# Optimization experiments

Hardware: AMD Instinct MI355X
Metric: run time of the kernel (lower is better)

## Reference

```python
import jax, jax.numpy as jnp
import numpy as np
from jax import lax

FS = 5
BL = np.array([1.46, 1.53, 1.33], np.float32)
BA = (np.pi - np.deg2rad(np.array([122.2, 111.9, 116.2]))).astype(np.float32)
A_SIN = (BL * np.sin(BA)).astype(np.float32)   # bond_length * sin(bond_angle)
A_COS = (BL * np.cos(BA)).astype(np.float32)   # bond_length * cos(bond_angle)
INIT_POS = np.array([[-np.sqrt(0.5), np.sqrt(1.5), 0.0],
                     [-np.sqrt(2.0), 0.0, 0.0],
                     [0.0, 0.0, 0.0]], np.float32)


def _rotation(pos):
    # pos: (..., 3 points, 3 coords); builds rot with columns (m_hat, n_hat x m_hat, n_hat)
    m0 = pos[..., 1, :] - pos[..., 0, :]
    m1 = pos[..., 2, :] - pos[..., 1, :]
    m_hat = m1 / (jnp.linalg.norm(m1, axis=-1, keepdims=True) + 1e-16)
    n = jnp.cross(m0, m_hat)
    n_hat = n / (jnp.linalg.norm(n, axis=-1, keepdims=True) + 1e-16)
    c = jnp.cross(n_hat, m_hat)
    return jnp.stack([m_hat, c, n_hat], axis=-1)


def _fragment_access(indices_np, fs=FS):
    # exact translation of PositionLookup.fragment index math (host-side, int constants)
    uniq, counts = np.unique(indices_np, return_counts=True)
    pad = (counts + fs - 1) // fs * fs
    last_pad = pad - counts
    off = np.roll(last_pad, 1)
    off[0] = 0
    off = np.repeat(off, counts)
    access = np.arange(counts.sum()) + off
    return access, int(pad.sum())


def _forward(torsions, access, P):
    # to_snr: (N,3) torsions -> (N, 3 atoms, 3 coords) local spherical points
    x = jnp.broadcast_to(jnp.asarray(A_COS), torsions.shape)
    points = jnp.stack([x, jnp.cos(torsions) * A_SIN, jnp.sin(torsions) * A_SIN], axis=-1)
    # fragment: scatter residues into padded per-chain slots
    padded = jnp.zeros((P, 3, 3), points.dtype).at[access].set(points)
    F = P // FS
    atom = padded.reshape(F, FS * 3, 3)          # (F, 15, 3) local snr points
    # stage 1: 15 sequential NeRF extension steps, vectorized over fragments
    pos0 = jnp.broadcast_to(jnp.asarray(INIT_POS), (F, 3, 3))
    def step(pos, d):                            # pos (F,3,3) last 3 atoms, d (F,3)
        rot = _rotation(pos)
        new = jnp.einsum('fij,fj->fi', rot, d) + pos[:, -1]
        return jnp.concatenate([pos[:, 1:], new[:, None]], axis=1), new
    _, atoms = lax.scan(step, pos0, jnp.swapaxes(atom, 0, 1))
    local = jnp.swapaxes(atoms, 0, 1)            # (F, 15, 3) fragment-local coords
    # stage 2: stitch fragments. Original right-to-left loop == exclusive prefix
    # composition of rigid transforms T_i built from fragment i's last 3 local atoms.
    rot_all = _rotation(local[:, -3:, :])        # (F,3,3)
    t_all = local[:, -1, :]                      # (F,3)
    eye = jnp.eye(3, dtype=local.dtype)[None]
    Rs = jnp.concatenate([eye, rot_all[:-1]], axis=0)
    ts = jnp.concatenate([jnp.zeros((1, 3), local.dtype), t_all[:-1]], axis=0)
    def combine(a, b):                           # (a o b)(x) = Ra(Rb x + tb) + ta
        Ra, ta = a
        Rb, tb = b
        return jnp.einsum('fij,fjk->fik', Ra, Rb), jnp.einsum('fij,fj->fi', Ra, tb) + ta
    Rp, tp = lax.associative_scan(combine, (Rs, ts))
    glob = jnp.einsum('fij,faj->fai', Rp, local) + tp[:, None, :]
    flat = glob.reshape(-1, 3)
    flat = flat - flat[:1]
    residues = flat.reshape(-1, 3, 3)            # (P//... , 3 atoms, 3 coords)
    return residues[jnp.asarray(access)]         # stitch: (N, 3, 3)


def setup_inputs():
    key = jax.random.key(0)
    n_chains, chain_len = 512, 2050              # chain_len % 5 == 0 -> zero padding
    N = n_chains * chain_len
    k1, _ = jax.random.split(key)
    torsions = jax.random.uniform(k1, (N, 3), jnp.float32, -np.pi, np.pi)
    indices = jnp.repeat(jnp.arange(n_chains, dtype=jnp.int32), chain_len)
    return {"torsions": torsions, "indices": indices}


def reference(torsions, indices):
    access, P = _fragment_access(np.asarray(indices))
    return _forward(torsions, access, P)
```

## Files before the change

kernel.cpp:

```cpp
#include <hip/hip_runtime.h>
#include <math.h>


struct Params {
    float as0, as1, as2;
    float ac0, ac1, ac2;
    float ip[9];
};

struct V3 { float x, y, z; };

__device__ __forceinline__ V3 v3(float x, float y, float z) { V3 r; r.x=x; r.y=y; r.z=z; return r; }
__device__ __forceinline__ V3 vsub(V3 a, V3 b) { return v3(a.x-b.x, a.y-b.y, a.z-b.z); }
__device__ __forceinline__ V3 vcross(V3 a, V3 b) {
    return v3(a.y*b.z - a.z*b.y, a.z*b.x - a.x*b.z, a.x*b.y - a.y*b.x);
}
__device__ __forceinline__ float vdot(V3 a, V3 b) { return a.x*b.x + a.y*b.y + a.z*b.z; }

struct Xform {
    float r[9];
    float t[3];
};

__device__ __forceinline__ Xform xf_identity() {
    Xform x;
    x.r[0]=1.f; x.r[1]=0.f; x.r[2]=0.f;
    x.r[3]=0.f; x.r[4]=1.f; x.r[5]=0.f;
    x.r[6]=0.f; x.r[7]=0.f; x.r[8]=1.f;
    x.t[0]=0.f; x.t[1]=0.f; x.t[2]=0.f;
    return x;
}

__device__ __forceinline__ Xform xf_compose(const Xform& a, const Xform& b) {
    Xform c;
#pragma unroll
    for (int i = 0; i < 3; ++i) {
#pragma unroll
        for (int j = 0; j < 3; ++j) {
            c.r[i*3+j] = a.r[i*3+0]*b.r[0*3+j] + a.r[i*3+1]*b.r[1*3+j] + a.r[i*3+2]*b.r[2*3+j];
        }
        c.t[i] = a.r[i*3+0]*b.t[0] + a.r[i*3+1]*b.t[1] + a.r[i*3+2]*b.t[2] + a.t[i];
    }
    return c;
}

__device__ __forceinline__ Xform xf_shfl_up(const Xform& x, int off) {
    Xform y;
#pragma unroll
    for (int i = 0; i < 9; ++i) y.r[i] = __shfl_up(x.r[i], off, 64);
#pragma unroll
    for (int i = 0; i < 3; ++i) y.t[i] = __shfl_up(x.t[i], off, 64);
    return y;
}
__device__ __forceinline__ Xform xf_shfl_down(const Xform& x, int off) {
    Xform y;
#pragma unroll
    for (int i = 0; i < 9; ++i) y.r[i] = __shfl_down(x.r[i], off, 64);
#pragma unroll
    for (int i = 0; i < 3; ++i) y.t[i] = __shfl_down(x.t[i], off, 64);
    return y;
}

#define LSTRIDE 13

__device__ __forceinline__ void xf_to_lds(float* p, const Xform& x) {
#pragma unroll
    for (int i = 0; i < 9; ++i) p[i] = x.r[i];
#pragma unroll
    for (int i = 0; i < 3; ++i) p[9+i] = x.t[i];
}
__device__ __forceinline__ Xform xf_from_lds(const float* p) {
    Xform x;
#pragma unroll
    for (int i = 0; i < 9; ++i) x.r[i] = p[i];
#pragma unroll
    for (int i = 0; i < 3; ++i) x.t[i] = p[9+i];
    return x;
}

__device__ __forceinline__ void xf_store_g(float* g, const Xform& x) {
    float4* q = (float4*)g;
    q[0] = make_float4(x.r[0], x.r[1], x.r[2], x.r[3]);
    q[1] = make_float4(x.r[4], x.r[5], x.r[6], x.r[7]);
    q[2] = make_float4(x.r[8], x.t[0], x.t[1], x.t[2]);
}
__device__ __forceinline__ Xform xf_load_g(const float* g) {
    const float4* q = (const float4*)g;
    float4 a = q[0], b = q[1], c = q[2];
    Xform x;
    x.r[0]=a.x; x.r[1]=a.y; x.r[2]=a.z; x.r[3]=a.w;
    x.r[4]=b.x; x.r[5]=b.y; x.r[6]=b.z; x.r[7]=b.w;
    x.r[8]=c.x; x.t[0]=c.y; x.t[1]=c.z; x.t[2]=c.w;
    return x;
}

__device__ __forceinline__ void fast_sincos(float t, float& s, float& c) {
    const float r = t * 0.15915494309189535f;
    s = __builtin_amdgcn_sinf(r);
    c = __builtin_amdgcn_cosf(r);
}

__device__ __forceinline__ void rot_cols(V3 p0, V3 p1, V3 p2, V3& mh, V3& cc, V3& nh) {
    V3 m0 = vsub(p1, p0);
    V3 m1 = vsub(p2, p1);
    float im = __builtin_amdgcn_rsqf(vdot(m1, m1));
    mh = v3(m1.x*im, m1.y*im, m1.z*im);
    V3 n = vcross(m0, mh);
    float il = __builtin_amdgcn_rsqf(vdot(n, n));
    nh = v3(n.x*il, n.y*il, n.z*il);
    cc = vcross(nh, mh);
}

template <bool STORE>
__device__ __forceinline__ void build_fragment(const float* __restrict__ tf, const Params& prm,
                                               V3* atoms, V3& q0, V3& q1, V3& q2) {
    V3 p0 = v3(prm.ip[0], prm.ip[1], prm.ip[2]);
    V3 p1 = v3(prm.ip[3], prm.ip[4], prm.ip[5]);
    V3 p2 = v3(prm.ip[6], prm.ip[7], prm.ip[8]);
    const float AS[3] = {prm.as0, prm.as1, prm.as2};
    const float AC[3] = {prm.ac0, prm.ac1, prm.ac2};
#pragma unroll
    for (int a = 0; a < 15; ++a) {
        const int j = a % 3;
        float s, c;
        fast_sincos(tf[a], s, c);
        V3 d = v3(AC[j], c * AS[j], s * AS[j]);
        V3 mh, cc, nh;
        rot_cols(p0, p1, p2, mh, cc, nh);
        V3 np;
        np.x = d.x*mh.x + d.y*cc.x + d.z*nh.x + p2.x;
        np.y = d.x*mh.y + d.y*cc.y + d.z*nh.y + p2.y;
        np.z = d.x*mh.z + d.y*cc.z + d.z*nh.z + p2.z;
        p0 = p1; p1 = p2; p2 = np;
        if (STORE) atoms[a] = np;
    }
    q0 = p0; q1 = p1; q2 = p2;
}

__device__ __forceinline__ Xform frag_transform(V3 q0, V3 q1, V3 q2) {
    V3 mh, cc, nh;
    rot_cols(q0, q1, q2, mh, cc, nh);
    Xform T;
    T.r[0]=mh.x; T.r[1]=cc.x; T.r[2]=nh.x;
    T.r[3]=mh.y; T.r[4]=cc.y; T.r[5]=nh.y;
    T.r[6]=mh.z; T.r[7]=cc.z; T.r[8]=nh.z;
    T.t[0]=q2.x; T.t[1]=q2.y; T.t[2]=q2.z;
    return T;
}

__global__ __launch_bounds__(256) void k_block_agg(const float* __restrict__ tors,
                                                   float* __restrict__ agg,
                                                   int F, Params prm) {
    __shared__ float tot[4 * LSTRIDE];
    const int tid = threadIdx.x;
    const int lane = tid & 63, w = tid >> 6;
    const long long f = (long long)blockIdx.x * 256 + tid;

    Xform T = xf_identity();
    if (f < F) {
        V3 q0, q1, q2;
        build_fragment<false>(tors + f * 15, prm, nullptr, q0, q1, q2);
        T = frag_transform(q0, q1, q2);
    }
#pragma unroll
    for (int off = 1; off < 64; off <<= 1) {
        Xform o = xf_shfl_down(T, off);
        T = xf_compose(T, o);
    }
    if (lane == 0) xf_to_lds(&tot[w * LSTRIDE], T);
    __syncthreads();
    if (tid == 0) {
        Xform A = xf_from_lds(&tot[0]);
#pragma unroll
        for (int j = 1; j < 4; ++j) A = xf_compose(A, xf_from_lds(&tot[j * LSTRIDE]));
        xf_store_g(agg + (size_t)blockIdx.x * 12, A);
    }
}

__global__ __launch_bounds__(256) void k_scan_agg(const float* __restrict__ agg,
                                                  float* __restrict__ pref, int nb) {
    __shared__ float tot[4 * LSTRIDE];
    const int t = threadIdx.x;
    const int lane = t & 63, w = t >> 6;

    Xform a[4];
#pragma unroll
    for (int k = 0; k < 4; ++k) {
        const int idx = t * 4 + k;
        a[k] = (idx < nb) ? xf_load_g(agg + (size_t)idx * 12) : xf_identity();
    }
    Xform T = xf_compose(xf_compose(a[0], a[1]), xf_compose(a[2], a[3]));
#pragma unroll
    for (int off = 1; off < 64; off <<= 1) {
        Xform o = xf_shfl_up(T, off);
        if (lane >= off) T = xf_compose(o, T);
    }
    if (lane == 63) xf_to_lds(&tot[w * LSTRIDE], T);
    __syncthreads();
    Xform E = xf_identity();
    for (int j = 0; j < w; ++j) E = xf_compose(E, xf_from_lds(&tot[j * LSTRIDE]));
    Xform S = xf_shfl_up(T, 1);
    if (lane > 0) E = xf_compose(E, S);
#pragma unroll
    for (int k = 0; k < 4; ++k) {
        const int idx = t * 4 + k;
        if (idx < nb) xf_store_g(pref + (size_t)idx * 12, E);
        E = xf_compose(E, a[k]);
    }
}

__global__ __launch_bounds__(256) void k_apply(const float* __restrict__ tors,
                                               const float* __restrict__ pref,
                                               float* __restrict__ out,
                                               int F, Params prm) {
    __shared__ __align__(16) float stage[256 * 45];
    __shared__ float tot[4 * LSTRIDE];
    const int tid = threadIdx.x;
    const int lane = tid & 63, w = tid >> 6;
    const long long f = (long long)blockIdx.x * 256 + tid;

    V3 atoms[15];
    Xform T = xf_identity();
    if (f < F) {
        V3 q0, q1, q2;
        build_fragment<true>(tors + f * 15, prm, atoms, q0, q1, q2);
        T = frag_transform(q0, q1, q2);
    }
#pragma unroll
    for (int off = 1; off < 64; off <<= 1) {
        Xform o = xf_shfl_up(T, off);
        if (lane >= off) T = xf_compose(o, T);
    }
    if (lane == 63) xf_to_lds(&tot[w * LSTRIDE], T);
    __syncthreads();

    Xform E = xf_load_g(pref + (size_t)blockIdx.x * 12);
    for (int j = 0; j < w; ++j) E = xf_compose(E, xf_from_lds(&tot[j * LSTRIDE]));
    Xform S = xf_shfl_up(T, 1);
    if (lane > 0) E = xf_compose(E, S);

    {
        float s0, c0;
        fast_sincos(tors[0], s0, c0);
        E.t[0] -= prm.ac0;
        E.t[1] -= c0 * prm.as0;
        E.t[2] -= s0 * prm.as0;
    }

    if (f < F) {
#pragma unroll
        for (int a = 0; a < 15; ++a) {
            V3 p = atoms[a];
            float gx = E.r[0]*p.x + E.r[1]*p.y + E.r[2]*p.z + E.t[0];
            float gy = E.r[3]*p.x + E.r[4]*p.y + E.r[5]*p.z + E.t[1];
            float gz = E.r[6]*p.x + E.r[7]*p.y + E.r[8]*p.z + E.t[2];
            stage[tid*45 + a*3 + 0] = gx;
            stage[tid*45 + a*3 + 1] = gy;
            stage[tid*45 + a*3 + 2] = gz;
        }
    }
    __syncthreads();

    const int nfrag = min(256, F - (int)blockIdx.x * 256);
    const size_t base = (size_t)blockIdx.x * 256 * 45;
    if (nfrag == 256) {
        float4* o4 = (float4*)(out + base);
        const float4* s4 = (const float4*)stage;
        for (int i = tid; i < (256 * 45) / 4; i += 256) o4[i] = s4[i];
    } else {
        const int total = nfrag * 45;
        for (int i = tid; i < total; i += 256) out[base + i] = stage[i];
    }
}

extern "C" void kernel_launch(void* const* d_in, const int* in_sizes, int n_in,
                              void* d_out, int out_size, void* d_ws, size_t ws_size,
                              hipStream_t stream) {
    const float* tors = (const float*)d_in[0];
    float* out = (float*)d_out;

    const int N = in_sizes[0] / 3;
    const int F = N / 5;
    const int nb = (F + 255) / 256;

    float* agg  = (float*)d_ws;
    float* pref = agg + (size_t)1024*12;

    Params P;
    {
        const double PI = 3.14159265358979323846;
        const double deg[3] = {122.2, 111.9, 116.2};
        const float  bl[3]  = {1.46f, 1.53f, 1.33f};
        for (int i = 0; i < 3; ++i) {
            float ba = (float)(PI - deg[i] * PI / 180.0);
            ((float*)&P.as0)[i] = (float)((double)bl[i] * sin((double)ba));
            ((float*)&P.ac0)[i] = (float)((double)bl[i] * cos((double)ba));
        }
        P.ip[0] = -(float)sqrt(0.5); P.ip[1] = (float)sqrt(1.5); P.ip[2] = 0.f;
        P.ip[3] = -(float)sqrt(2.0); P.ip[4] = 0.f;              P.ip[5] = 0.f;
        P.ip[6] = 0.f;               P.ip[7] = 0.f;              P.ip[8] = 0.f;
    }

    k_block_agg<<<nb, 256, 0, stream>>>(tors, agg, F, P);
    k_scan_agg<<<1, 256, 0, stream>>>(agg, pref, nb);
    k_apply<<<nb, 256, 0, stream>>>(tors, pref, out, F, P);
}
```

Before: 102.4 us.

## Track unit bond directions in NeRF, stage torsions in LDS, fold block scan into apply

The NeRF recurrence now carries the previous and current unit bond vectors and the running position, instead of three positions that are renormalized each step. This removes one rsqrt and the subtractions from each of the 15 steps, using a precomputed inverse bond length. Torsions are loaded into LDS with coalesced float4 reads before per-thread use, replacing strided per-thread global loads. The separate single-block prefix kernel is dropped: each apply block reduces all preceding block aggregates itself. That saves one launch but adds redundant work that grows with block index, and it may shift floating-point rounding.

```diff
diff --git a/kernel.cpp b/kernel.cpp
--- a/kernel.cpp
+++ b/kernel.cpp
@@ -5,22 +5,19 @@
 struct Params {
     float as0, as1, as2;
     float ac0, ac1, ac2;
-    float ip[9];
+    float ibl0, ibl1, ibl2;
+    float upx, upy, upz;
 };
 
 struct V3 { float x, y, z; };
 
 __device__ __forceinline__ V3 v3(float x, float y, float z) { V3 r; r.x=x; r.y=y; r.z=z; return r; }
-__device__ __forceinline__ V3 vsub(V3 a, V3 b) { return v3(a.x-b.x, a.y-b.y, a.z-b.z); }
 __device__ __forceinline__ V3 vcross(V3 a, V3 b) {
     return v3(a.y*b.z - a.z*b.y, a.z*b.x - a.x*b.z, a.x*b.y - a.y*b.x);
 }
 __device__ __forceinline__ float vdot(V3 a, V3 b) { return a.x*b.x + a.y*b.y + a.z*b.z; }
 
-struct Xform {
-    float r[9];
-    float t[3];
-};
+struct Xform { float r[9]; float t[3]; };
 
 __device__ __forceinline__ Xform xf_identity() {
     Xform x;
@@ -36,9 +33,8 @@
 #pragma unroll
     for (int i = 0; i < 3; ++i) {
 #pragma unroll
-        for (int j = 0; j < 3; ++j) {
+        for (int j = 0; j < 3; ++j)
             c.r[i*3+j] = a.r[i*3+0]*b.r[0*3+j] + a.r[i*3+1]*b.r[1*3+j] + a.r[i*3+2]*b.r[2*3+j];
-        }
         c.t[i] = a.r[i*3+0]*b.t[0] + a.r[i*3+1]*b.t[1] + a.r[i*3+2]*b.t[2] + a.t[i];
     }
     return c;
@@ -100,73 +96,85 @@
     c = __builtin_amdgcn_cosf(r);
 }
 
-__device__ __forceinline__ void rot_cols(V3 p0, V3 p1, V3 p2, V3& mh, V3& cc, V3& nh) {
-    V3 m0 = vsub(p1, p0);
-    V3 m1 = vsub(p2, p1);
-    float im = __builtin_amdgcn_rsqf(vdot(m1, m1));
-    mh = v3(m1.x*im, m1.y*im, m1.z*im);
-    V3 n = vcross(m0, mh);
-    float il = __builtin_amdgcn_rsqf(vdot(n, n));
-    nh = v3(n.x*il, n.y*il, n.z*il);
-    cc = vcross(nh, mh);
-}
-
 template <bool STORE>
 __device__ __forceinline__ void build_fragment(const float* __restrict__ tf, const Params& prm,
-                                               V3* atoms, V3& q0, V3& q1, V3& q2) {
-    V3 p0 = v3(prm.ip[0], prm.ip[1], prm.ip[2]);
-    V3 p1 = v3(prm.ip[3], prm.ip[4], prm.ip[5]);
-    V3 p2 = v3(prm.ip[6], prm.ip[7], prm.ip[8]);
-    const float AS[3] = {prm.as0, prm.as1, prm.as2};
-    const float AC[3] = {prm.ac0, prm.ac1, prm.ac2};
+                                               V3* atoms, V3& up_o, V3& u_o, V3& p_o) {
+    V3 up = v3(prm.upx, prm.upy, prm.upz);
+    V3 u  = v3(1.f, 0.f, 0.f);
+    V3 p  = v3(0.f, 0.f, 0.f);
+    const float AS[3]  = {prm.as0,  prm.as1,  prm.as2};
+    const float AC[3]  = {prm.ac0,  prm.ac1,  prm.ac2};
+    const float IBL[3] = {prm.ibl0, prm.ibl1, prm.ibl2};
 #pragma unroll
     for (int a = 0; a < 15; ++a) {
         const int j = a % 3;
         float s, c;
         fast_sincos(tf[a], s, c);
-        V3 d = v3(AC[j], c * AS[j], s * AS[j]);
-        V3 mh, cc, nh;
-        rot_cols(p0, p1, p2, mh, cc, nh);
-        V3 np;
-        np.x = d.x*mh.x + d.y*cc.x + d.z*nh.x + p2.x;
-        np.y = d.x*mh.y + d.y*cc.y + d.z*nh.y + p2.y;
-        np.z = d.x*mh.z + d.y*cc.z + d.z*nh.z + p2.z;
-        p0 = p1; p1 = p2; p2 = np;
-        if (STORE) atoms[a] = np;
-    }
-    q0 = p0; q1 = p1; q2 = p2;
-}
-
-__device__ __forceinline__ Xform frag_transform(V3 q0, V3 q1, V3 q2) {
-    V3 mh, cc, nh;
-    rot_cols(q0, q1, q2, mh, cc, nh);
+        V3 n = vcross(up, u);
+        float il = __builtin_amdgcn_rsqf(vdot(n, n));
+        V3 nh = v3(n.x*il, n.y*il, n.z*il);
+        V3 cc = vcross(nh, u);
+        const float dy = c * AS[j], dz = s * AS[j];
+        V3 w;
+        w.x = AC[j]*u.x + dy*cc.x + dz*nh.x;
+        w.y = AC[j]*u.y + dy*cc.y + dz*nh.y;
+        w.z = AC[j]*u.z + dy*cc.z + dz*nh.z;
+        p = v3(p.x + w.x, p.y + w.y, p.z + w.z);
+        up = u;
+        u = v3(w.x*IBL[j], w.y*IBL[j], w.z*IBL[j]);
+        if (STORE) atoms[a] = p;
+    }
+    up_o = up; u_o = u; p_o = p;
+}
+
+__device__ __forceinline__ Xform frag_transform(V3 up, V3 u, V3 p) {
+    V3 n = vcross(up, u);
+    float il = __builtin_amdgcn_rsqf(vdot(n, n));
+    V3 nh = v3(n.x*il, n.y*il, n.z*il);
+    V3 cc = vcross(nh, u);
     Xform T;
-    T.r[0]=mh.x; T.r[1]=cc.x; T.r[2]=nh.x;
-    T.r[3]=mh.y; T.r[4]=cc.y; T.r[5]=nh.y;
-    T.r[6]=mh.z; T.r[7]=cc.z; T.r[8]=nh.z;
-    T.t[0]=q2.x; T.t[1]=q2.y; T.t[2]=q2.z;
+    T.r[0]=u.x; T.r[1]=cc.x; T.r[2]=nh.x;
+    T.r[3]=u.y; T.r[4]=cc.y; T.r[5]=nh.y;
+    T.r[6]=u.z; T.r[7]=cc.z; T.r[8]=nh.z;
+    T.t[0]=p.x; T.t[1]=p.y; T.t[2]=p.z;
     return T;
+}
+
+__device__ __forceinline__ void wave_reduce(Xform& T) {
+#pragma unroll
+    for (int off = 1; off < 64; off <<= 1) {
+        Xform o = xf_shfl_down(T, off);
+        T = xf_compose(T, o);
+    }
 }
 
 __global__ __launch_bounds__(256) void k_block_agg(const float* __restrict__ tors,
                                                    float* __restrict__ agg,
                                                    int F, Params prm) {
+    __shared__ __align__(16) float tslab[256 * 15];
     __shared__ float tot[4 * LSTRIDE];
     const int tid = threadIdx.x;
     const int lane = tid & 63, w = tid >> 6;
-    const long long f = (long long)blockIdx.x * 256 + tid;
+    const int f0 = blockIdx.x * 256;
+    const int nfrag = min(256, F - f0);
+
+    if (nfrag == 256) {
+        const float4* tg = (const float4*)(tors + (size_t)f0 * 15);
+        float4* ts4 = (float4*)tslab;
+        for (int i = tid; i < 960; i += 256) ts4[i] = tg[i];
+    } else {
+        const int total = nfrag * 15;
+        for (int i = tid; i < total; i += 256) tslab[i] = tors[(size_t)f0 * 15 + i];
+    }
+    __syncthreads();
 
     Xform T = xf_identity();
-    if (f < F) {
-        V3 q0, q1, q2;
-        build_fragment<false>(tors + f * 15, prm, nullptr, q0, q1, q2);
-        T = frag_transform(q0, q1, q2);
-    }
-#pragma unroll
-    for (int off = 1; off < 64; off <<= 1) {
-        Xform o = xf_shfl_down(T, off);
-        T = xf_compose(T, o);
-    }
+    if (tid < nfrag) {
+        V3 up, u, p;
+        build_fragment<false>(&tslab[tid * 15], prm, nullptr, up, u, p);
+        T = frag_transform(up, u, p);
+    }
+    wave_reduce(T);
     if (lane == 0) xf_to_lds(&tot[w * LSTRIDE], T);
     __syncthreads();
     if (tid == 0) {
@@ -177,65 +185,66 @@
     }
 }
 
-__global__ __launch_bounds__(256) void k_scan_agg(const float* __restrict__ agg,
-                                                  float* __restrict__ pref, int nb) {
-    __shared__ float tot[4 * LSTRIDE];
-    const int t = threadIdx.x;
-    const int lane = t & 63, w = t >> 6;
-
-    Xform a[4];
-#pragma unroll
-    for (int k = 0; k < 4; ++k) {
-        const int idx = t * 4 + k;
-        a[k] = (idx < nb) ? xf_load_g(agg + (size_t)idx * 12) : xf_identity();
-    }
-    Xform T = xf_compose(xf_compose(a[0], a[1]), xf_compose(a[2], a[3]));
+__global__ __launch_bounds__(256) void k_apply(const float* __restrict__ tors,
+                                               const float* __restrict__ agg,
+                                               float* __restrict__ out,
+                                               int F, Params prm) {
+    __shared__ __align__(16) float stage[256 * 45];
+    __shared__ float totA[4 * LSTRIDE];
+    __shared__ float totB[4 * LSTRIDE];
+    __shared__ float bcast[12];
+    const int tid = threadIdx.x;
+    const int lane = tid & 63, w = tid >> 6;
+    const int b = blockIdx.x;
+    const int f0 = b * 256;
+    const int nfrag = min(256, F - f0);
+
+    if (nfrag == 256) {
+        const float4* tg = (const float4*)(tors + (size_t)f0 * 15);
+        float4* ts4 = (float4*)stage;
+        for (int i = tid; i < 960; i += 256) ts4[i] = tg[i];
+    } else {
+        const int total = nfrag * 15;
+        for (int i = tid; i < total; i += 256) stage[i] = tors[(size_t)f0 * 15 + i];
+    }
+    __syncthreads();
+
+    V3 atoms[15];
+    Xform T = xf_identity();
+    V3 up, u, p;
+    if (tid < nfrag) {
+        build_fragment<true>(&stage[tid * 15], prm, atoms, up, u, p);
+        T = frag_transform(up, u, p);
+    }
+
+    Xform R = xf_identity();
+    {
+        const int g = (b + 255) >> 8;
+        if (g) {
+            const int s = tid * g;
+            const int e = min(s + g, b);
+            for (int k = s; k < e; ++k) R = xf_compose(R, xf_load_g(agg + (size_t)k * 12));
+        }
+        wave_reduce(R);
+    }
 #pragma unroll
     for (int off = 1; off < 64; off <<= 1) {
         Xform o = xf_shfl_up(T, off);
         if (lane >= off) T = xf_compose(o, T);
     }
-    if (lane == 63) xf_to_lds(&tot[w * LSTRIDE], T);
-    __syncthreads();
-    Xform E = xf_identity();
-    for (int j = 0; j < w; ++j) E = xf_compose(E, xf_from_lds(&tot[j * LSTRIDE]));
-    Xform S = xf_shfl_up(T, 1);
-    if (lane > 0) E = xf_compose(E, S);
-#pragma unroll
-    for (int k = 0; k < 4; ++k) {
-        const int idx = t * 4 + k;
-        if (idx < nb) xf_store_g(pref + (size_t)idx * 12, E);
-        E = xf_compose(E, a[k]);
-    }
-}
-
-__global__ __launch_bounds__(256) void k_apply(const float* __restrict__ tors,
-                                               const float* __restrict__ pref,
-                                               float* __restrict__ out,
-                                               int F, Params prm) {
-    __shared__ __align__(16) float stage[256 * 45];
-    __shared__ float tot[4 * LSTRIDE];
-    const int tid = threadIdx.x;
-    const int lane = tid & 63, w = tid >> 6;
-    const long long f = (long long)blockIdx.x * 256 + tid;
-
-    V3 atoms[15];
-    Xform T = xf_identity();
-    if (f < F) {
-        V3 q0, q1, q2;
-        build_fragment<true>(tors + f * 15, prm, atoms, q0, q1, q2);
-        T = frag_transform(q0, q1, q2);
-    }
-#pragma unroll
-    for (int off = 1; off < 64; off <<= 1) {
-        Xform o = xf_shfl_up(T, off);
-        if (lane >= off) T = xf_compose(o, T);
-    }
-    if (lane == 63) xf_to_lds(&tot[w * LSTRIDE], T);
-    __syncthreads();
-
-    Xform E = xf_load_g(pref + (size_t)blockIdx.x * 12);
-    for (int j = 0; j < w; ++j) E = xf_compose(E, xf_from_lds(&tot[j * LSTRIDE]));
+    if (lane == 0)  xf_to_lds(&totB[w * LSTRIDE], R);
+    if (lane == 63) xf_to_lds(&totA[w * LSTRIDE], T);
+    __syncthreads();
+    if (tid == 0) {
+        Xform Eb = xf_from_lds(&totB[0]);
+#pragma unroll
+        for (int j = 1; j < 4; ++j) Eb = xf_compose(Eb, xf_from_lds(&totB[j * LSTRIDE]));
+        xf_to_lds(bcast, Eb);
+    }
+    __syncthreads();
+
+    Xform E = xf_from_lds(bcast);
+    for (int j = 0; j < w; ++j) E = xf_compose(E, xf_from_lds(&totA[j * LSTRIDE]));
     Xform S = xf_shfl_up(T, 1);
     if (lane > 0) E = xf_compose(E, S);
 
@@ -247,13 +256,13 @@
         E.t[2] -= s0 * prm.as0;
     }
 
-    if (f < F) {
+    if (tid < nfrag) {
 #pragma unroll
         for (int a = 0; a < 15; ++a) {
-            V3 p = atoms[a];
-            float gx = E.r[0]*p.x + E.r[1]*p.y + E.r[2]*p.z + E.t[0];
-            float gy = E.r[3]*p.x + E.r[4]*p.y + E.r[5]*p.z + E.t[1];
-            float gz = E.r[6]*p.x + E.r[7]*p.y + E.r[8]*p.z + E.t[2];
+            V3 q = atoms[a];
+            float gx = E.r[0]*q.x + E.r[1]*q.y + E.r[2]*q.z + E.t[0];
+            float gy = E.r[3]*q.x + E.r[4]*q.y + E.r[5]*q.z + E.t[1];
+            float gz = E.r[6]*q.x + E.r[7]*q.y + E.r[8]*q.z + E.t[2];
             stage[tid*45 + a*3 + 0] = gx;
             stage[tid*45 + a*3 + 1] = gy;
             stage[tid*45 + a*3 + 2] = gz;
@@ -261,8 +270,7 @@
     }
     __syncthreads();
 
-    const int nfrag = min(256, F - (int)blockIdx.x * 256);
-    const size_t base = (size_t)blockIdx.x * 256 * 45;
+    const size_t base = (size_t)b * 256 * 45;
     if (nfrag == 256) {
         float4* o4 = (float4*)(out + base);
         const float4* s4 = (const float4*)stage;
@@ -283,25 +291,25 @@
     const int F = N / 5;
     const int nb = (F + 255) / 256;
 
-    float* agg  = (float*)d_ws;
-    float* pref = agg + (size_t)1024*12;
+    float* agg = (float*)d_ws;
 
     Params P;
     {
         const double PI = 3.14159265358979323846;
         const double deg[3] = {122.2, 111.9, 116.2};
-        const float  bl[3]  = {1.46f, 1.53f, 1.33f};
+        const double bl[3]  = {1.46, 1.53, 1.33};
+        float* as_ = &P.as0; float* ac_ = &P.ac0; float* ib_ = &P.ibl0;
         for (int i = 0; i < 3; ++i) {
-            float ba = (float)(PI - deg[i] * PI / 180.0);
-            ((float*)&P.as0)[i] = (float)((double)bl[i] * sin((double)ba));
-            ((float*)&P.ac0)[i] = (float)((double)bl[i] * cos((double)ba));
+            double ba = PI - deg[i] * PI / 180.0;
+            float baf = (float)ba;
+            float blf = (float)bl[i];
+            as_[i] = (float)((double)blf * sin((double)baf));
+            ac_[i] = (float)((double)blf * cos((double)baf));
+            ib_[i] = 1.0f / blf;
         }
-        P.ip[0] = -(float)sqrt(0.5); P.ip[1] = (float)sqrt(1.5); P.ip[2] = 0.f;
-        P.ip[3] = -(float)sqrt(2.0); P.ip[4] = 0.f;              P.ip[5] = 0.f;
-        P.ip[6] = 0.f;               P.ip[7] = 0.f;              P.ip[8] = 0.f;
+        P.upx = -0.5f; P.upy = -0.8660254037844386f; P.upz = 0.f;
     }
 
     k_block_agg<<<nb, 256, 0, stream>>>(tors, agg, F, P);
-    k_scan_agg<<<1, 256, 0, stream>>>(agg, pref, nb);
-    k_apply<<<nb, 256, 0, stream>>>(tors, pref, out, F, P);
-}
+    k_apply<<<nb, 256, 0, stream>>>(tors, agg, out, F, P);
+}
```

New measurement: 98.96 us. -3.3%, faster.
